# Optimization experiments

Measured on AMD Instinct MI355X. Metric: run time of the kernel, lower is better.

The kernel has to match this reference:

```python
import jax, jax.numpy as jnp
import numpy as np

EPS = 1e-5
HEADS = 16
DIM_HEAD = 64
ROPE_THETA = 10000.0


def layer_norm(x, g, b):
    mu = x.mean(-1, keepdims=True)
    var = x.var(-1, keepdims=True)
    return (x - mu) / jnp.sqrt(var + EPS) * g + b


def apply_rope(t):
    # t: [b, h, n, d]; interleaved-pair RoPE (rotary-embedding-torch default)
    n, d = t.shape[-2], t.shape[-1]
    inv_freq = 1.0 / (ROPE_THETA ** (jnp.arange(0, d, 2, dtype=jnp.float32) / d))  # [d/2]
    freqs = jnp.arange(n, dtype=jnp.float32)[:, None] * inv_freq[None, :]          # [n, d/2]
    freqs = jnp.repeat(freqs, 2, axis=-1)                                          # [n, d]
    cos, sin = jnp.cos(freqs).astype(t.dtype), jnp.sin(freqs).astype(t.dtype)
    t2 = t.reshape(*t.shape[:-1], d // 2, 2)
    t_rot = jnp.stack((-t2[..., 1], t2[..., 0]), axis=-1).reshape(t.shape)
    return t * cos + t_rot * sin


def setup_inputs() -> dict:
    key = jax.random.key(0)
    k0, k1, k2 = jax.random.split(key, 3)
    B, N, D = 1, 4096, 1024
    inner = HEADS * DIM_HEAD
    x = jax.random.normal(k0, (B, N, D), jnp.float32)
    w_qkv = jax.random.normal(k1, (D, inner * 3), jnp.float32) * (D ** -0.5)
    w_out = jax.random.normal(k2, (inner, D), jnp.float32) * (inner ** -0.5)
    ln_g = jnp.ones((D,), jnp.float32)
    ln_b = jnp.zeros((D,), jnp.float32)
    return {"x": x, "w_qkv": w_qkv, "w_out": w_out, "ln_g": ln_g, "ln_b": ln_b}


def reference(x, w_qkv, w_out, ln_g, ln_b):
    B, N, D = x.shape
    H, DH = HEADS, DIM_HEAD
    scale = DH ** -0.5

    h = layer_norm(x, ln_g, ln_b)
    qkv = h @ w_qkv                                    # [b, n, 3*inner]
    q, k, v = jnp.split(qkv, 3, axis=-1)
    to_heads = lambda t: t.reshape(B, N, H, DH).transpose(0, 2, 1, 3)  # [b,h,n,d]
    q, k, v = to_heads(q), to_heads(k), to_heads(v)

    new_k, new_v = k, v  # cache holds pre-RoPE k, v (as in original)

    q = apply_rope(q)
    k = apply_rope(k)

    dots = jnp.einsum('bhid,bhjd->bhij', q, k) * scale  # [b,h,n,n]
    causal_mask = jnp.triu(jnp.ones((N, N), dtype=bool), 1)
    dots = jnp.where(causal_mask, -jnp.inf, dots)
    attn = jax.nn.softmax(dots, axis=-1)
    out = jnp.einsum('bhij,bhjd->bhid', attn, v)        # [b,h,n,d]
    out = out.transpose(0, 2, 1, 3).reshape(B, N, H * DH)
    return out @ w_out, new_k, new_v
```

## Files before the change

### kernel.cpp

```cpp
#include <hip/hip_runtime.h>
#include <math.h>

#define D_MODEL 1024
#define N_SEQ   4096
#define N_HEADS 16
#define DHEAD   64
#define QKV_COLS 3072

typedef short bf16x8 __attribute__((ext_vector_type(8)));
typedef short bf16x4 __attribute__((ext_vector_type(4)));
typedef float f32x4  __attribute__((ext_vector_type(4)));

#define MFMA32(a, b, c) __builtin_amdgcn_mfma_f32_16x16x32_bf16(a, b, c, 0, 0, 0)
#define MFMA16(a, b, c) __builtin_amdgcn_mfma_f32_16x16x16bf16_1k(a, b, c, 0, 0, 0)

static __device__ __forceinline__ unsigned short f2bf(float f) {
    union { float f; unsigned u; } v; v.f = f;
    unsigned r = (v.u + 0x7fffu + ((v.u >> 16) & 1u)) >> 16;
    return (unsigned short)r;
}

static __device__ __forceinline__ bf16x4 pack_bf16x4(float a, float b, float c, float d) {
    union { float f; unsigned u; } x0, x1, x2, x3;
    x0.f = a; x1.f = b; x2.f = c; x3.f = d;
    union { unsigned u[2]; bf16x4 v; } r;
    r.u[0] = __builtin_amdgcn_perm(x1.u, x0.u, 0x07060302u);
    r.u[1] = __builtin_amdgcn_perm(x3.u, x2.u, 0x07060302u);
    return r.v;
}

typedef __attribute__((address_space(1))) const void* gas_t;
typedef __attribute__((address_space(3))) void* las_t;
static __device__ __forceinline__ void load_lds16(const unsigned short* g, unsigned short* l) {
    __builtin_amdgcn_global_load_lds((gas_t)g, (las_t)l, 16, 0, 0);
}

__global__ __launch_bounds__(256) void ln_kernel(const float* __restrict__ x,
                                                 const float* __restrict__ g,
                                                 const float* __restrict__ b,
                                                 unsigned short* __restrict__ h) {
    int row = blockIdx.x;
    int t = threadIdx.x;
    float4 v = ((const float4*)(x + (size_t)row * D_MODEL))[t];
    float s  = v.x + v.y + v.z + v.w;
    float ss = v.x*v.x + v.y*v.y + v.z*v.z + v.w*v.w;
    for (int off = 32; off; off >>= 1) {
        s  += __shfl_down(s, off);
        ss += __shfl_down(ss, off);
    }
    __shared__ float sm[4], ssm[4];
    __shared__ float mu_s, rs_s;
    int wave = t >> 6, lane = t & 63;
    if (lane == 0) { sm[wave] = s; ssm[wave] = ss; }
    __syncthreads();
    if (t == 0) {
        float S = 0.f, SS = 0.f;
        for (int w = 0; w < 4; w++) { S += sm[w]; SS += ssm[w]; }
        float mu = S / D_MODEL;
        float var = SS / D_MODEL - mu * mu;
        mu_s = mu;
        rs_s = rsqrtf(var + 1e-5f);
    }
    __syncthreads();
    float mu = mu_s, rs = rs_s;
    float4 gv = ((const float4*)g)[t];
    float4 bv = ((const float4*)b)[t];
    ushort4 o;
    o.x = f2bf((v.x - mu) * rs * gv.x + bv.x);
    o.y = f2bf((v.y - mu) * rs * gv.y + bv.y);
    o.z = f2bf((v.z - mu) * rs * gv.z + bv.z);
    o.w = f2bf((v.w - mu) * rs * gv.w + bv.w);
    *(ushort4*)(h + (size_t)row * D_MODEL + t * 4) = o;
}

__global__ __launch_bounds__(256) void transpose_cvt(const float* __restrict__ W,
                                                     unsigned short* __restrict__ Wt,
                                                     int K, int N) {
    __shared__ float tile[64][65];
    int k0 = blockIdx.x * 64, n0 = blockIdx.y * 64;
    int t = threadIdx.x;
#pragma unroll
    for (int p = 0; p < 16; p++) {
        int idx = p * 256 + t;
        int r = idx >> 6, c = idx & 63;
        tile[r][c] = W[(size_t)(k0 + r) * N + n0 + c];
    }
    __syncthreads();
#pragma unroll
    for (int p = 0; p < 16; p++) {
        int idx = p * 256 + t;
        int r2 = idx >> 6, c2 = idx & 63;
        Wt[(size_t)(n0 + r2) * K + k0 + c2] = f2bf(tile[c2][r2]);
    }
}

__global__ __launch_bounds__(256) void gemm_bt128(const unsigned short* __restrict__ A,
                                                  const unsigned short* __restrict__ Bt,
                                                  float* __restrict__ C,
                                                  int M, int N, int K) {
    __shared__ unsigned short As[128 * 32];
    __shared__ unsigned short Bs[128 * 32];
    int t = threadIdx.x;
    int w = t >> 6, lane = t & 63;
    int l16 = lane & 15, quad = lane >> 4;
    int wr = w >> 1, wc = w & 1;
    int m0 = blockIdx.x * 128, n0 = blockIdx.y * 128;
    int srow = lane >> 2, scol = (lane & 3) * 8;
    int c0 = w * 2, c1 = c0 + 1;

    f32x4 acc[4][4] = {};

    for (int k0 = 0; k0 < K; k0 += 32) {
        __syncthreads();
        load_lds16(A  + (size_t)(m0 + c0 * 16 + srow) * K + k0 + scol, &As[c0 * 512 + lane * 8]);
        load_lds16(A  + (size_t)(m0 + c1 * 16 + srow) * K + k0 + scol, &As[c1 * 512 + lane * 8]);
        load_lds16(Bt + (size_t)(n0 + c0 * 16 + srow) * K + k0 + scol, &Bs[c0 * 512 + lane * 8]);
        load_lds16(Bt + (size_t)(n0 + c1 * 16 + srow) * K + k0 + scol, &Bs[c1 * 512 + lane * 8]);
        __syncthreads();
        bf16x8 a[4], b[4];
#pragma unroll
        for (int mt = 0; mt < 4; mt++)
            a[mt] = *(const bf16x8*)&As[(wr * 64 + mt * 16 + l16) * 32 + quad * 8];
#pragma unroll
        for (int nt = 0; nt < 4; nt++)
            b[nt] = *(const bf16x8*)&Bs[(wc * 64 + nt * 16 + l16) * 32 + quad * 8];
#pragma unroll
        for (int mt = 0; mt < 4; mt++)
#pragma unroll
            for (int nt = 0; nt < 4; nt++)
                acc[mt][nt] = MFMA32(a[mt], b[nt], acc[mt][nt]);
    }
#pragma unroll
    for (int mt = 0; mt < 4; mt++)
#pragma unroll
        for (int nt = 0; nt < 4; nt++)
#pragma unroll
            for (int r = 0; r < 4; r++)
                C[(size_t)(m0 + wr * 64 + mt * 16 + quad * 4 + r) * N + n0 + wc * 64 + nt * 16 + l16] =
                    acc[mt][nt][r];
}

__global__ __launch_bounds__(256) void rope_cache_kernel(const float* __restrict__ qkv,
                                                         float* __restrict__ out_k,
                                                         float* __restrict__ out_v,
                                                         unsigned short* __restrict__ q_bf,
                                                         unsigned short* __restrict__ k_bf,
                                                         unsigned short* __restrict__ vt_bf) {
    __shared__ unsigned short Vt[64 * 72];
    int nt = blockIdx.x, h = blockIdx.y;
    int n0 = nt * 64;
    int t = threadIdx.x;
    int row = t >> 2;
    int n = n0 + row;
    const float* src = qkv + (size_t)n * QKV_COLS + h * 64;
    size_t nd_base = ((size_t)h * N_SEQ + n) * 64;
#pragma unroll
    for (int j = 0; j < 4; j++) {
        int c = (t & 3) * 4 + j * 16;
        float4 q4 = *(const float4*)(src + c);
        float4 k4 = *(const float4*)(src + 1024 + c);
        float4 v4 = *(const float4*)(src + 2048 + c);
        *(float4*)(out_k + nd_base + c) = k4;
        *(float4*)(out_v + nd_base + c) = v4;
        float i0 = (float)(c >> 1), i1 = i0 + 1.f;
        float if0 = powf(10000.0f, -i0 / 32.0f);
        float if1 = powf(10000.0f, -i1 / 32.0f);
        float s0, c0s, s1, c1s;
        sincosf((float)n * if0, &s0, &c0s);
        sincosf((float)n * if1, &s1, &c1s);
        ushort4 qo, ko;
        qo.x = f2bf(q4.x * c0s - q4.y * s0); qo.y = f2bf(q4.y * c0s + q4.x * s0);
        qo.z = f2bf(q4.z * c1s - q4.w * s1); qo.w = f2bf(q4.w * c1s + q4.z * s1);
        ko.x = f2bf(k4.x * c0s - k4.y * s0); ko.y = f2bf(k4.y * c0s + k4.x * s0);
        ko.z = f2bf(k4.z * c1s - k4.w * s1); ko.w = f2bf(k4.w * c1s + k4.z * s1);
        *(ushort4*)(q_bf + nd_base + c) = qo;
        *(ushort4*)(k_bf + nd_base + c) = ko;
        ushort4 vo;
        vo.x = f2bf(v4.x); vo.y = f2bf(v4.y); vo.z = f2bf(v4.z); vo.w = f2bf(v4.w);
        *(ushort4*)&Vt[row * 72 + c] = vo;
    }
    __syncthreads();
    int d = t >> 2;
    int nb = (t & 3) * 16;
    unsigned short tmp[16];
#pragma unroll
    for (int i = 0; i < 16; i++) tmp[i] = Vt[(nb + i) * 72 + d];
    unsigned short* dst = vt_bf + ((size_t)h * DHEAD + d) * N_SEQ + n0 + nb;
#pragma unroll
    for (int i = 0; i < 16; i++) dst[i] = tmp[i];
}

__global__ __launch_bounds__(256, 4) void flash_mfma(const unsigned short* __restrict__ q_bf,
                                                     const unsigned short* __restrict__ k_bf,
                                                     const unsigned short* __restrict__ vt_bf,
                                                     unsigned short* __restrict__ attn_bf,
                                                     float* __restrict__ part_O,
                                                     float* __restrict__ part_l) {
    int idx = blockIdx.x;
    int h = idx & 15;
    int u = idx >> 4;
    int Qt, cc;
    bool partial = (u < 72);
    if (partial) {
        int r = 71 - u;
        if (r < 16)      { Qt = 8 + (r >> 1); cc = r & 1; }
        else if (r < 40) { int q3 = r - 16; int d3 = q3 / 3; Qt = 16 + d3; cc = q3 - 3 * d3; }
        else             { int q4 = r - 40; Qt = 24 + (q4 >> 2); cc = q4 & 3; }
    } else { Qt = 79 - u; cc = 0; }
    int kt0 = cc * 16;
    int kt_end = min(kt0 + 15, 2 * Qt + 1);

    int t = threadIdx.x;
    int w = t >> 6, lane = t & 63;
    int l16 = lane & 15, quad = lane >> 4;
    int sw = l16 & 7;

    __shared__ unsigned short Ks[64 * 64];
    __shared__ unsigned short Vs[64 * 64];

    int qr0 = Qt * 128 + w * 32;
    const unsigned short* Kg = k_bf + (size_t)h * N_SEQ * DHEAD;
    const unsigned short* Vg = vt_bf + (size_t)h * DHEAD * N_SEQ;

    bf16x8 bq[2][2];
#pragma unroll
    for (int qg = 0; qg < 2; qg++) {
        const unsigned short* qp = q_bf + ((size_t)h * N_SEQ + qr0 + qg * 16 + l16) * 64 + quad * 8;
        bq[qg][0] = *(const bf16x8*)(qp);
        bq[qg][1] = *(const bf16x8*)(qp + 32);
    }
    f32x4 O[2][4] = {};
    float lp[2] = {0.f, 0.f};
    int my_kmax = (qr0 + 31) >> 6;

    int srow = t >> 3;
    int scol = ((t & 7) ^ (srow & 7)) * 8;
    const float CEXP = 0.18033688011112042f;

    for (int kt = kt0; kt <= kt_end; kt++) {
        int k0 = kt << 6;
        __syncthreads();
        load_lds16(Kg + (size_t)(k0 + srow) * 64 + scol,         &Ks[t * 8]);
        load_lds16(Kg + (size_t)(k0 + srow + 32) * 64 + scol,    &Ks[t * 8 + 2048]);
        load_lds16(Vg + (size_t)srow * N_SEQ + k0 + scol,        &Vs[t * 8]);
        load_lds16(Vg + (size_t)(srow + 32) * N_SEQ + k0 + scol, &Vs[t * 8 + 2048]);
        __syncthreads();
        if (kt > my_kmax) continue;

        bf16x4 pf[2][4];
#pragma unroll
        for (int tt = 0; tt < 4; tt++) {
            int kbase = k0 + tt * 16;
            bf16x4 pz = (bf16x4){0, 0, 0, 0};
            if (kbase >= qr0 + 32) { pf[0][tt] = pz; pf[1][tt] = pz; continue; }
            int krow = tt * 16 + l16;
            bf16x8 kf0 = *(const bf16x8*)&Ks[krow * 64 + ((quad ^ sw) * 8)];
            bf16x8 kf1 = *(const bf16x8*)&Ks[krow * 64 + (((quad + 4) ^ sw) * 8)];
#pragma unroll
            for (int qg = 0; qg < 2; qg++) {
                int qb = qr0 + qg * 16;
                if (kbase > qb) { pf[qg][tt] = pz; continue; }
                f32x4 s = (f32x4){0.f, 0.f, 0.f, 0.f};
                s = MFMA32(kf0, bq[qg][0], s);
                s = MFMA32(kf1, bq[qg][1], s);
                float p0 = exp2f(s[0] * CEXP);
                float p1 = exp2f(s[1] * CEXP);
                float p2 = exp2f(s[2] * CEXP);
                float p3 = exp2f(s[3] * CEXP);
                if (kbase == qb) {
                    if (quad * 4 + 0 > l16) p0 = 0.f;
                    if (quad * 4 + 1 > l16) p1 = 0.f;
                    if (quad * 4 + 2 > l16) p2 = 0.f;
                    if (quad * 4 + 3 > l16) p3 = 0.f;
                }
                lp[qg] += (p0 + p1) + (p2 + p3);
                pf[qg][tt] = pack_bf16x4(p0, p1, p2, p3);
            }
        }
#pragma unroll
        for (int tt = 0; tt < 4; tt++) {
            if (k0 + tt * 16 < qr0 + 32) {
#pragma unroll
                for (int dt = 0; dt < 4; dt++) {
                    int vrow = dt * 16 + l16;
                    bf16x4 va = *(const bf16x4*)&Vs[vrow * 64 +
                                (((2 * tt + (quad >> 1)) ^ sw) * 8) + (quad & 1) * 4];
                    O[0][dt] = MFMA16(va, pf[0][tt], O[0][dt]);
                    O[1][dt] = MFMA16(va, pf[1][tt], O[1][dt]);
                }
            }
        }
    }

#pragma unroll
    for (int qg = 0; qg < 2; qg++) {
        float l = lp[qg];
        l += __shfl_xor(l, 16);
        l += __shfl_xor(l, 32);
        if (!partial) {
            float inv = 1.0f / l;
#pragma unroll
            for (int dt = 0; dt < 4; dt++) {
                ushort4 o;
                o.x = f2bf(O[qg][dt][0] * inv);
                o.y = f2bf(O[qg][dt][1] * inv);
                o.z = f2bf(O[qg][dt][2] * inv);
                o.w = f2bf(O[qg][dt][3] * inv);
                *(ushort4*)(attn_bf + (size_t)(qr0 + qg * 16 + l16) * D_MODEL + h * 64 + dt * 16 + quad * 4) = o;
            }
        } else {
            int uid = h * 72 + u;
            size_t ob = (size_t)uid * 8192;
            int qcol = w * 32 + qg * 16 + l16;
#pragma unroll
            for (int dt = 0; dt < 4; dt++)
#pragma unroll
                for (int r = 0; r < 4; r++)
                    part_O[ob + (size_t)(dt * 16 + quad * 4 + r) * 128 + qcol] = O[qg][dt][r];
            if (quad == 0) part_l[uid * 128 + qcol] = l;
        }
    }
}

__global__ __launch_bounds__(256) void combine_kernel(const float* __restrict__ part_O,
                                                      const float* __restrict__ part_l,
                                                      unsigned short* __restrict__ attn_bf) {
    int Qt = 8 + blockIdx.x;
    int h  = blockIdx.y;
    int nc = (Qt + 8) >> 3;
    int t = threadIdx.x;
    int q = t & 127;
    int dh = (t >> 7) * 32;
    float l = 0.f;
    float acc[32];
#pragma unroll
    for (int d = 0; d < 32; d++) acc[d] = 0.f;
    for (int c = 0; c < nc; c++) {
        int r;
        if (Qt < 16)      r = 2 * (Qt - 8) + c;
        else if (Qt < 24) r = 16 + 3 * (Qt - 16) + c;
        else              r = 40 + 4 * (Qt - 24) + c;
        int uid = h * 72 + (71 - r);
        l += part_l[uid * 128 + q];
        const float* po = part_O + (size_t)uid * 8192 + (size_t)dh * 128 + q;
#pragma unroll
        for (int d = 0; d < 32; d++) acc[d] += po[d * 128];
    }
    float inv = 1.0f / l;
    unsigned short* op = attn_bf + (size_t)(Qt * 128 + q) * D_MODEL + h * 64 + dh;
#pragma unroll
    for (int d = 0; d < 32; d++) op[d] = f2bf(acc[d] * inv);
}

extern "C" void kernel_launch(void* const* d_in, const int* in_sizes, int n_in,
                              void* d_out, int out_size, void* d_ws, size_t ws_size,
                              hipStream_t stream) {
    const float* x     = (const float*)d_in[0];
    const float* w_qkv = (const float*)d_in[1];
    const float* w_out = (const float*)d_in[2];
    const float* ln_g  = (const float*)d_in[3];
    const float* ln_b  = (const float*)d_in[4];

    float* out   = (float*)d_out;
    float* out_k = (float*)d_out + 4194304;
    float* out_v = (float*)d_out + 8388608;

    char* ws = (char*)d_ws;
    const size_t MiB = 1048576;
    float*          qkv_f   = (float*)(ws);
    unsigned short* h_bf    = (unsigned short*)(ws + 48*MiB);
    unsigned short* wqkvT   = (unsigned short*)(ws + 56*MiB);
    unsigned short* q_bf    = (unsigned short*)(ws + 48*MiB);
    unsigned short* k_bf    = (unsigned short*)(ws + 56*MiB);
    unsigned short* vt_bf   = (unsigned short*)(ws + 64*MiB);
    unsigned short* attn_bf = (unsigned short*)(ws);
    float*          part_l  = (float*)(ws + 8*MiB);
    float*          part_O  = (float*)(ws + 9*MiB);
    unsigned short* woutT   = (unsigned short*)(ws + 72*MiB);

    transpose_cvt<<<dim3(16, 48), 256, 0, stream>>>(w_qkv, wqkvT, D_MODEL, QKV_COLS);
    transpose_cvt<<<dim3(16, 16), 256, 0, stream>>>(w_out, woutT, D_MODEL, D_MODEL);
    ln_kernel<<<N_SEQ, 256, 0, stream>>>(x, ln_g, ln_b, h_bf);
    gemm_bt128<<<dim3(32, 24), 256, 0, stream>>>(h_bf, wqkvT, qkv_f, N_SEQ, QKV_COLS, D_MODEL);
    rope_cache_kernel<<<dim3(64, 16), 256, 0, stream>>>(qkv_f, out_k, out_v, q_bf, k_bf, vt_bf);
    flash_mfma<<<1280, 256, 0, stream>>>(q_bf, k_bf, vt_bf, attn_bf, part_O, part_l);
    combine_kernel<<<dim3(24, 16), 256, 0, stream>>>(part_O, part_l, attn_bf);
    gemm_bt128<<<dim3(32, 8), 256, 0, stream>>>(attn_bf, woutT, out, N_SEQ, D_MODEL, D_MODEL);
}
```

Baseline: 272.3 us.

## Double-buffer K/V tiles in LDS and compute row sums with MFMA

The flash attention loop now uses two LDS buffers for K and V. The next tile's global-to-LDS load is issued right after a single barrier, so it overlaps compute on the current tile, and the second barrier per iteration is gone. The softmax denominator now comes from an extra MFMA against a ones vector instead of scalar adds and cross-lane shuffles, and LDS offsets are precomputed once outside the loop. The PV MFMA section runs at raised wave priority via s_setprio. Occupancy is lowered from 4 to 3 blocks per CU to make room for the doubled shared memory and the extra registers.

```diff
diff --git a/kernel.cpp b/kernel.cpp
--- a/kernel.cpp
+++ b/kernel.cpp
@@ -190,7 +190,7 @@
     for (int i = 0; i < 16; i++) dst[i] = tmp[i];
 }
 
-__global__ __launch_bounds__(256, 4) void flash_mfma(const unsigned short* __restrict__ q_bf,
+__global__ __launch_bounds__(256, 3) void flash_mfma(const unsigned short* __restrict__ q_bf,
                                                      const unsigned short* __restrict__ k_bf,
                                                      const unsigned short* __restrict__ vt_bf,
                                                      unsigned short* __restrict__ attn_bf,
@@ -215,8 +215,8 @@
     int l16 = lane & 15, quad = lane >> 4;
     int sw = l16 & 7;
 
-    __shared__ unsigned short Ks[64 * 64];
-    __shared__ unsigned short Vs[64 * 64];
+    __shared__ unsigned short Ks[2][4096];
+    __shared__ unsigned short Vs[2][4096];
 
     int qr0 = Qt * 128 + w * 32;
     const unsigned short* Kg = k_bf + (size_t)h * N_SEQ * DHEAD;
@@ -230,22 +230,53 @@
         bq[qg][1] = *(const bf16x8*)(qp + 32);
     }
     f32x4 O[2][4] = {};
-    float lp[2] = {0.f, 0.f};
+    f32x4 Ol[2] = {};
     int my_kmax = (qr0 + 31) >> 6;
 
     int srow = t >> 3;
     int scol = ((t & 7) ^ (srow & 7)) * 8;
     const float CEXP = 0.18033688011112042f;
 
-    for (int kt = kt0; kt <= kt_end; kt++) {
+    int koffA[4], koffB[4];
+#pragma unroll
+    for (int tt = 0; tt < 4; tt++) {
+        int krow = tt * 16 + l16;
+        koffA[tt] = krow * 64 + ((quad ^ sw) * 8);
+        koffB[tt] = krow * 64 + (((quad + 4) ^ sw) * 8);
+    }
+    int voff[4][4];
+#pragma unroll
+    for (int tt = 0; tt < 4; tt++)
+#pragma unroll
+        for (int dt = 0; dt < 4; dt++)
+            voff[tt][dt] = (dt * 16 + l16) * 64 +
+                           (((2 * tt + (quad >> 1)) ^ sw) * 8) + (quad & 1) * 4;
+
+    const unsigned short* kg0 = Kg + (size_t)(kt0 * 64 + srow) * 64 + scol;
+    const unsigned short* kg1 = kg0 + 2048;
+    const unsigned short* vg0 = Vg + (size_t)srow * N_SEQ + kt0 * 64 + scol;
+    const unsigned short* vg1 = vg0 + (size_t)32 * N_SEQ;
+
+    const bf16x4 ones4 = {(short)0x3F80, (short)0x3F80, (short)0x3F80, (short)0x3F80};
+
+    load_lds16(kg0, &Ks[0][t * 8]);
+    load_lds16(kg1, &Ks[0][t * 8 + 2048]);
+    load_lds16(vg0, &Vs[0][t * 8]);
+    load_lds16(vg1, &Vs[0][t * 8 + 2048]);
+    kg0 += 4096; kg1 += 4096; vg0 += 64; vg1 += 64;
+
+    auto step = [&](int kt, const unsigned short* KC, const unsigned short* VC,
+                    unsigned short* KN, unsigned short* VN) {
+        __syncthreads();
+        if (kt < kt_end) {
+            load_lds16(kg0, KN + t * 8);
+            load_lds16(kg1, KN + t * 8 + 2048);
+            load_lds16(vg0, VN + t * 8);
+            load_lds16(vg1, VN + t * 8 + 2048);
+            kg0 += 4096; kg1 += 4096; vg0 += 64; vg1 += 64;
+        }
+        if (kt > my_kmax) return;
         int k0 = kt << 6;
-        __syncthreads();
-        load_lds16(Kg + (size_t)(k0 + srow) * 64 + scol,         &Ks[t * 8]);
-        load_lds16(Kg + (size_t)(k0 + srow + 32) * 64 + scol,    &Ks[t * 8 + 2048]);
-        load_lds16(Vg + (size_t)srow * N_SEQ + k0 + scol,        &Vs[t * 8]);
-        load_lds16(Vg + (size_t)(srow + 32) * N_SEQ + k0 + scol, &Vs[t * 8 + 2048]);
-        __syncthreads();
-        if (kt > my_kmax) continue;
 
         bf16x4 pf[2][4];
 #pragma unroll
@@ -253,9 +284,8 @@
             int kbase = k0 + tt * 16;
             bf16x4 pz = (bf16x4){0, 0, 0, 0};
             if (kbase >= qr0 + 32) { pf[0][tt] = pz; pf[1][tt] = pz; continue; }
-            int krow = tt * 16 + l16;
-            bf16x8 kf0 = *(const bf16x8*)&Ks[krow * 64 + ((quad ^ sw) * 8)];
-            bf16x8 kf1 = *(const bf16x8*)&Ks[krow * 64 + (((quad + 4) ^ sw) * 8)];
+            bf16x8 kf0 = *(const bf16x8*)&KC[koffA[tt]];
+            bf16x8 kf1 = *(const bf16x8*)&KC[koffB[tt]];
 #pragma unroll
             for (int qg = 0; qg < 2; qg++) {
                 int qb = qr0 + qg * 16;
@@ -273,30 +303,34 @@
                     if (quad * 4 + 2 > l16) p2 = 0.f;
                     if (quad * 4 + 3 > l16) p3 = 0.f;
                 }
-                lp[qg] += (p0 + p1) + (p2 + p3);
                 pf[qg][tt] = pack_bf16x4(p0, p1, p2, p3);
+                Ol[qg] = MFMA16(ones4, pf[qg][tt], Ol[qg]);
             }
         }
+        __builtin_amdgcn_s_setprio(1);
 #pragma unroll
         for (int tt = 0; tt < 4; tt++) {
             if (k0 + tt * 16 < qr0 + 32) {
 #pragma unroll
                 for (int dt = 0; dt < 4; dt++) {
-                    int vrow = dt * 16 + l16;
-                    bf16x4 va = *(const bf16x4*)&Vs[vrow * 64 +
-                                (((2 * tt + (quad >> 1)) ^ sw) * 8) + (quad & 1) * 4];
+                    bf16x4 va = *(const bf16x4*)&VC[voff[tt][dt]];
                     O[0][dt] = MFMA16(va, pf[0][tt], O[0][dt]);
                     O[1][dt] = MFMA16(va, pf[1][tt], O[1][dt]);
                 }
             }
         }
+        __builtin_amdgcn_s_setprio(0);
+    };
+
+    for (int kt = kt0; kt <= kt_end; ) {
+        step(kt, Ks[0], Vs[0], Ks[1], Vs[1]); kt++;
+        if (kt > kt_end) break;
+        step(kt, Ks[1], Vs[1], Ks[0], Vs[0]); kt++;
     }
 
 #pragma unroll
     for (int qg = 0; qg < 2; qg++) {
-        float l = lp[qg];
-        l += __shfl_xor(l, 16);
-        l += __shfl_xor(l, 32);
+        float l = Ol[qg][0];
         if (!partial) {
             float inv = 1.0f / l;
 #pragma unroll
```

Result: no change. 269.6 us (-1.0%).
